# Performance work log

Measured on AMD Instinct MI355X. Metric: run time of the kernel, lower is better.

Reference implementation:

```python
import jax, jax.numpy as jnp
import numpy as np

N_NODES = 8192
N_EDGES = 8192
DEG = 32          # nodes per hyperedge
NNZ = N_EDGES * DEG
D = 32            # embedding_dim / hidden_channels


def setup_inputs() -> dict:
    key = jax.random.key(0)
    ks = jax.random.split(key, 12)
    x_0 = jax.random.normal(ks[0], (N_NODES, D), dtype=jnp.float32)
    # incidence structure: each hyperedge touches DEG random nodes
    node_idx = jax.random.randint(ks[1], (NNZ,), 0, N_NODES)
    edge_idx = jnp.repeat(jnp.arange(N_EDGES), DEG)
    incidence_1 = jnp.zeros((N_NODES, N_EDGES), jnp.float32).at[node_idx, edge_idx].set(1.0)
    s = 1.0 / np.sqrt(D)
    # UniGCN layer weights (level-2 conv linear transform per layer, 2 layers)
    W_l1 = jax.random.uniform(ks[2], (D, D), jnp.float32, -s, s)
    W_l2 = jax.random.uniform(ks[3], (D, D), jnp.float32, -s, s)
    # 3-layer MLP (Linear(64,32), Linear(32,32), Linear(32,1)), no activations
    s2 = 1.0 / np.sqrt(2 * D)
    Wm1 = jax.random.uniform(ks[4], (2 * D, D), jnp.float32, -s2, s2)
    bm1 = jax.random.uniform(ks[5], (D,), jnp.float32, -s2, s2)
    Wm2 = jax.random.uniform(ks[6], (D, D), jnp.float32, -s, s)
    bm2 = jax.random.uniform(ks[7], (D,), jnp.float32, -s, s)
    Wm3 = jax.random.uniform(ks[8], (D, 1), jnp.float32, -s, s)
    bm3 = jax.random.uniform(ks[9], (1,), jnp.float32, -s, s)
    return {"x_0": x_0, "incidence_1": incidence_1,
            "W_l1": W_l1, "W_l2": W_l2,
            "Wm1": Wm1, "bm1": bm1, "Wm2": Wm2, "bm2": bm2,
            "Wm3": Wm3, "bm3": bm3,
            "node_idx": node_idx, "edge_idx": edge_idx}


def _unigcn(x_0, inc, W_l1, W_l2):
    # UniGCN layer: level1 (0->1, no linear transform), level2 (1->0, linear)
    x_1 = inc.T @ x_0                 # [E, D]
    x_0 = inc @ (x_1 @ W_l1)          # [N, D]
    x_1 = inc.T @ x_0                 # [E, D]
    x_0 = inc @ (x_1 @ W_l2)          # [N, D]
    return x_0, x_1


def reference(x_0, incidence_1, W_l1, W_l2, Wm1, bm1, Wm2, bm2, Wm3, bm3,
              node_idx, edge_idx):
    x_0_new, x_1_new = _unigcn(x_0, incidence_1, W_l1, W_l2)
    # gather embeddings at incidence nonzeros
    h = jnp.concatenate([x_0_new[node_idx], x_1_new[edge_idx]], axis=1)  # [NNZ, 2D]
    h = h @ Wm1 + bm1
    h = h @ Wm2 + bm2
    vals = (h @ Wm3 + bm3)[:, 0]                                          # [NNZ]
    # scatter back into dense [N, E] matrix
    output_counts = jnp.zeros_like(incidence_1).at[node_idx, edge_idx].set(vals)
    return output_counts
```

## Files before the change

### kernel.cpp

```cpp
#include <hip/hip_runtime.h>

#define N_NODES 8192
#define N_EDGES 8192
#define DEG 32
#define D 32
#define CAP 128
#define FILL_GRID 2048

typedef float vf4 __attribute__((ext_vector_type(4)));


__global__ void __launch_bounds__(256)
k1_fill(const float* __restrict__ x0, const float* __restrict__ Wl1,
        const float* __restrict__ Wl2, const float* __restrict__ Wm1,
        const float* __restrict__ bm1, const float* __restrict__ Wm2,
        const float* __restrict__ bm2, const float* __restrict__ Wm3,
        const float* __restrict__ bm3, const int* __restrict__ node_idx,
        float* __restrict__ A, unsigned* __restrict__ validmask,
        int* __restrict__ cursor, int* __restrict__ csr_e,
        float* __restrict__ consts, float* __restrict__ out) {
    const int t = threadIdx.x, el = t >> 5, s = t & 31;

    if (blockIdx.x < N_EDGES / 8) {
        __shared__ int sidx[8][32];
        __shared__ unsigned smask[8];
        __shared__ float fsh[128];
        if (blockIdx.x == 0) {
            float* w23 = fsh;
            float* M0  = fsh + 32;
            float* M1  = fsh + 64;
            float* w2u = fsh + 96;
            if (t < 32) {
                float acc = 0.f;
                for (int k = 0; k < 32; ++k) acc += Wm2[t * 32 + k] * Wm3[k];
                w23[t] = acc;
            }
            __syncthreads();
            if (t < 64) {
                float acc = 0.f;
                for (int k = 0; k < 32; ++k) acc += Wm1[t * 32 + k] * w23[k];
                if (t < 32) M0[t] = acc; else M1[t - 32] = acc;
            }
            if (t == 0) {
                float c = bm3[0];
                for (int k = 0; k < 32; ++k) c += bm1[k] * w23[k] + bm2[k] * Wm3[k];
                consts[0] = c;
            }
            __syncthreads();
            if (t < 32) {
                float acc = 0.f;
                for (int d2 = 0; d2 < 32; ++d2) acc += Wl2[t * 32 + d2] * M0[d2];
                w2u[t] = acc;
            }
            __syncthreads();
            if (t < 32) {
                float ay = 0.f, az = 0.f;
                for (int d2 = 0; d2 < 32; ++d2) {
                    float w = Wl1[t * 32 + d2];
                    ay += w * w2u[d2];
                    az += w * M1[d2];
                }
                consts[1 + t]  = ay;
                consts[33 + t] = az;
            }
            __syncthreads();
        }

        int e = blockIdx.x * 8 + el;
        int idx = node_idx[e * DEG + s];
        sidx[el][s] = idx;
        __syncthreads();
        bool valid = true;
        for (int j = 0; j < s; ++j)
            if (sidx[el][j] == idx) { valid = false; break; }
        unsigned long long bl = __ballot(valid);
        if (s == 0) {
            unsigned m = (unsigned)(bl >> (t & 32));
            smask[el] = m;
            validmask[e] = m;
        }
        if (valid) {
            int pos = atomicAdd(&cursor[idx], 1);
            if (pos < CAP) csr_e[idx * CAP + pos] = e;
        }
        __syncthreads();
        unsigned m = smask[el];
        float acc = 0.f;
#pragma unroll
        for (int j = 0; j < 32; ++j)
            if ((m >> j) & 1u) acc += x0[sidx[el][j] * D + s];
        A[e * D + s] = acc;
    }

    vf4* dst = (vf4*)out;
    const long long nvec = (long long)N_NODES * N_EDGES / 4;
    const long long stride = (long long)FILL_GRID * 256;
    vf4 zz = (vf4)(0.f);
    for (long long i = (long long)blockIdx.x * 256 + t; i < nvec; i += stride)
        dst[i] = zz;
}

__global__ void __launch_bounds__(256)
k2_node(const float* __restrict__ A, const int* __restrict__ csr_e,
        const int* __restrict__ cursor, const float* __restrict__ consts,
        float* __restrict__ y, float* __restrict__ z) {
    const int t = threadIdx.x, el = t >> 5, s = t & 31;
    int n = blockIdx.x * 8 + el;
    int cnt = min(cursor[n], CAP);
    const int* lst = csr_e + n * CAP;
    float acc = 0.f;
    int j = 0;
    for (; j + 4 <= cnt; j += 4) {
        int4 e4 = *(const int4*)(lst + j);
        acc += A[e4.x * D + s] + A[e4.y * D + s] +
               A[e4.z * D + s] + A[e4.w * D + s];
    }
    for (; j < cnt; ++j) acc += A[lst[j] * D + s];
    float ay = acc * consts[1 + s];
    float az = acc * consts[33 + s];
#pragma unroll
    for (int off = 16; off; off >>= 1) {
        ay += __shfl_xor(ay, off);
        az += __shfl_xor(az, off);
    }
    if (s == 0) { y[n] = ay; z[n] = az; }
}

__global__ void __launch_bounds__(256)
k2_edge(const int* __restrict__ node_idx, const unsigned* __restrict__ validmask,
        const float* __restrict__ y, const float* __restrict__ z,
        float* __restrict__ qw, float* __restrict__ q) {
    const int t = threadIdx.x, el = t >> 5, s = t & 31;
    int e = blockIdx.x * 8 + el;
    unsigned m = validmask[e];
    int idx = node_idx[e * DEG + s];
    bool valid = (m >> s) & 1u;
    float ay = valid ? y[idx] : 0.f;
    float az = valid ? z[idx] : 0.f;
#pragma unroll
    for (int off = 16; off; off >>= 1) {
        ay += __shfl_xor(ay, off);
        az += __shfl_xor(az, off);
    }
    if (s == 0) { qw[e] = ay; q[e] = az; }
}

__global__ void __launch_bounds__(256)
k_patch(const int* __restrict__ csr_e, const int* __restrict__ cursor,
        const float* __restrict__ qw, const float* __restrict__ q,
        const float* __restrict__ consts, float* __restrict__ out) {
    const int t = threadIdx.x, el = t >> 5, s = t & 31;
    int n = blockIdx.x * 8 + el;
    int cnt = min(cursor[n], CAP);
    const int* lst = csr_e + n * CAP;
    float acc = 0.f;
    for (int j = s; j < cnt; j += 32) acc += qw[lst[j]];
#pragma unroll
    for (int off = 16; off; off >>= 1) acc += __shfl_xor(acc, off);
    float pn = acc + consts[0];
    float* rowp = out + (size_t)n * N_EDGES;
    for (int j = s; j < cnt; j += 32) {
        int e = lst[j];
        rowp[e] = pn + q[e];
    }
}

extern "C" void kernel_launch(void* const* d_in, const int* in_sizes, int n_in,
                              void* d_out, int out_size, void* d_ws, size_t ws_size,
                              hipStream_t stream) {
    const float* x0  = (const float*)d_in[0];
    const float* Wl1 = (const float*)d_in[2];
    const float* Wl2 = (const float*)d_in[3];
    const float* Wm1 = (const float*)d_in[4];
    const float* bm1 = (const float*)d_in[5];
    const float* Wm2 = (const float*)d_in[6];
    const float* bm2 = (const float*)d_in[7];
    const float* Wm3 = (const float*)d_in[8];
    const float* bm3 = (const float*)d_in[9];
    const int* node_idx = (const int*)d_in[10];
    float* out = (float*)d_out;

    char* ws = (char*)d_ws;
    int*      cursor    = (int*)(ws);
    float*    y         = (float*)(ws + ( 32u << 10));
    float*    z         = (float*)(ws + ( 64u << 10));
    unsigned* validmask = (unsigned*)(ws + ( 96u << 10));
    float*    qw        = (float*)(ws + (128u << 10));
    float*    q         = (float*)(ws + (160u << 10));
    float*    consts    = (float*)(ws + (192u << 10));
    float*    A         = (float*)(ws + (1u << 20));
    int*      csr_e     = (int*)(ws + (2u << 20));

    hipMemsetAsync(cursor, 0, N_NODES * sizeof(int), stream);
    k1_fill<<<FILL_GRID, 256, 0, stream>>>(x0, Wl1, Wl2, Wm1, bm1, Wm2, bm2,
                                           Wm3, bm3, node_idx, A, validmask,
                                           cursor, csr_e, consts, out);
    k2_node<<<N_NODES / 8, 256, 0, stream>>>(A, csr_e, cursor, consts, y, z);
    k2_edge<<<N_EDGES / 8, 256, 0, stream>>>(node_idx, validmask, y, z, qw, q);
    k_patch<<<N_NODES / 8, 256, 0, stream>>>(csr_e, cursor, qw, q, consts, out);
}
```

Before: 82.40 us.

## Move output zero-fill from first kernel into per-row patch kernel

The dense 256MB output zero-fill is moved out of the first kernel, where it ran grid-strided alongside the edge/CSR work. It now lives in the final patch kernel, where each block zeroes 4 full rows and then scatters the nonzero values into those same rows. Rows are written while still hot in cache, and the first kernel becomes a small edge-only launch. The cost is that the fill no longer overlaps the edge, node and edge-reduce stages, and only 4 of 8 warps do the patch work.

```diff
diff --git a/kernel.cpp b/kernel.cpp
--- a/kernel.cpp
+++ b/kernel.cpp
@@ -5,99 +5,90 @@
 #define DEG 32
 #define D 32
 #define CAP 128
-#define FILL_GRID 2048
+#define ROWS_PER_BLK 4
 
 typedef float vf4 __attribute__((ext_vector_type(4)));
 
 
 __global__ void __launch_bounds__(256)
-k1_fill(const float* __restrict__ x0, const float* __restrict__ Wl1,
+k1_edge(const float* __restrict__ x0, const float* __restrict__ Wl1,
         const float* __restrict__ Wl2, const float* __restrict__ Wm1,
         const float* __restrict__ bm1, const float* __restrict__ Wm2,
         const float* __restrict__ bm2, const float* __restrict__ Wm3,
         const float* __restrict__ bm3, const int* __restrict__ node_idx,
         float* __restrict__ A, unsigned* __restrict__ validmask,
         int* __restrict__ cursor, int* __restrict__ csr_e,
-        float* __restrict__ consts, float* __restrict__ out) {
+        float* __restrict__ consts) {
+    __shared__ int sidx[8][32];
+    __shared__ unsigned smask[8];
+    __shared__ float fsh[128];
     const int t = threadIdx.x, el = t >> 5, s = t & 31;
 
-    if (blockIdx.x < N_EDGES / 8) {
-        __shared__ int sidx[8][32];
-        __shared__ unsigned smask[8];
-        __shared__ float fsh[128];
-        if (blockIdx.x == 0) {
-            float* w23 = fsh;
-            float* M0  = fsh + 32;
-            float* M1  = fsh + 64;
-            float* w2u = fsh + 96;
-            if (t < 32) {
-                float acc = 0.f;
-                for (int k = 0; k < 32; ++k) acc += Wm2[t * 32 + k] * Wm3[k];
-                w23[t] = acc;
+    if (blockIdx.x == 0) {
+        float* w23 = fsh;
+        float* M0  = fsh + 32;
+        float* M1  = fsh + 64;
+        float* w2u = fsh + 96;
+        if (t < 32) {
+            float acc = 0.f;
+            for (int k = 0; k < 32; ++k) acc += Wm2[t * 32 + k] * Wm3[k];
+            w23[t] = acc;
+        }
+        __syncthreads();
+        if (t < 64) {
+            float acc = 0.f;
+            for (int k = 0; k < 32; ++k) acc += Wm1[t * 32 + k] * w23[k];
+            if (t < 32) M0[t] = acc; else M1[t - 32] = acc;
+        }
+        if (t == 0) {
+            float c = bm3[0];
+            for (int k = 0; k < 32; ++k) c += bm1[k] * w23[k] + bm2[k] * Wm3[k];
+            consts[0] = c;
+        }
+        __syncthreads();
+        if (t < 32) {
+            float acc = 0.f;
+            for (int d2 = 0; d2 < 32; ++d2) acc += Wl2[t * 32 + d2] * M0[d2];
+            w2u[t] = acc;
+        }
+        __syncthreads();
+        if (t < 32) {
+            float ay = 0.f, az = 0.f;
+            for (int d2 = 0; d2 < 32; ++d2) {
+                float w = Wl1[t * 32 + d2];
+                ay += w * w2u[d2];
+                az += w * M1[d2];
             }
-            __syncthreads();
-            if (t < 64) {
-                float acc = 0.f;
-                for (int k = 0; k < 32; ++k) acc += Wm1[t * 32 + k] * w23[k];
-                if (t < 32) M0[t] = acc; else M1[t - 32] = acc;
-            }
-            if (t == 0) {
-                float c = bm3[0];
-                for (int k = 0; k < 32; ++k) c += bm1[k] * w23[k] + bm2[k] * Wm3[k];
-                consts[0] = c;
-            }
-            __syncthreads();
-            if (t < 32) {
-                float acc = 0.f;
-                for (int d2 = 0; d2 < 32; ++d2) acc += Wl2[t * 32 + d2] * M0[d2];
-                w2u[t] = acc;
-            }
-            __syncthreads();
-            if (t < 32) {
-                float ay = 0.f, az = 0.f;
-                for (int d2 = 0; d2 < 32; ++d2) {
-                    float w = Wl1[t * 32 + d2];
-                    ay += w * w2u[d2];
-                    az += w * M1[d2];
-                }
-                consts[1 + t]  = ay;
-                consts[33 + t] = az;
-            }
-            __syncthreads();
-        }
-
-        int e = blockIdx.x * 8 + el;
-        int idx = node_idx[e * DEG + s];
-        sidx[el][s] = idx;
-        __syncthreads();
-        bool valid = true;
-        for (int j = 0; j < s; ++j)
-            if (sidx[el][j] == idx) { valid = false; break; }
-        unsigned long long bl = __ballot(valid);
-        if (s == 0) {
-            unsigned m = (unsigned)(bl >> (t & 32));
-            smask[el] = m;
-            validmask[e] = m;
-        }
-        if (valid) {
-            int pos = atomicAdd(&cursor[idx], 1);
-            if (pos < CAP) csr_e[idx * CAP + pos] = e;
-        }
-        __syncthreads();
-        unsigned m = smask[el];
-        float acc = 0.f;
-#pragma unroll
-        for (int j = 0; j < 32; ++j)
-            if ((m >> j) & 1u) acc += x0[sidx[el][j] * D + s];
-        A[e * D + s] = acc;
-    }
-
-    vf4* dst = (vf4*)out;
-    const long long nvec = (long long)N_NODES * N_EDGES / 4;
-    const long long stride = (long long)FILL_GRID * 256;
-    vf4 zz = (vf4)(0.f);
-    for (long long i = (long long)blockIdx.x * 256 + t; i < nvec; i += stride)
-        dst[i] = zz;
+            consts[1 + t]  = ay;
+            consts[33 + t] = az;
+        }
+        __syncthreads();
+    }
+
+    int e = blockIdx.x * 8 + el;
+    int idx = node_idx[e * DEG + s];
+    sidx[el][s] = idx;
+    __syncthreads();
+    bool valid = true;
+    for (int j = 0; j < s; ++j)
+        if (sidx[el][j] == idx) { valid = false; break; }
+    unsigned long long bl = __ballot(valid);
+    if (s == 0) {
+        unsigned m = (unsigned)(bl >> (t & 32));
+        smask[el] = m;
+        validmask[e] = m;
+    }
+    if (valid) {
+        int pos = atomicAdd(&cursor[idx], 1);
+        if (pos < CAP) csr_e[idx * CAP + pos] = e;
+    }
+    __syncthreads();
+    unsigned m = smask[el];
+    float acc = 0.f;
+#pragma unroll
+    for (int j = 0; j < 32; ++j)
+        if ((m >> j) & 1u) acc += x0[sidx[el][j] * D + s];
+    A[e * D + s] = acc;
 }
 
 __global__ void __launch_bounds__(256)
@@ -146,22 +137,33 @@
 }
 
 __global__ void __launch_bounds__(256)
-k_patch(const int* __restrict__ csr_e, const int* __restrict__ cursor,
-        const float* __restrict__ qw, const float* __restrict__ q,
-        const float* __restrict__ consts, float* __restrict__ out) {
-    const int t = threadIdx.x, el = t >> 5, s = t & 31;
-    int n = blockIdx.x * 8 + el;
-    int cnt = min(cursor[n], CAP);
-    const int* lst = csr_e + n * CAP;
-    float acc = 0.f;
-    for (int j = s; j < cnt; j += 32) acc += qw[lst[j]];
-#pragma unroll
-    for (int off = 16; off; off >>= 1) acc += __shfl_xor(acc, off);
-    float pn = acc + consts[0];
-    float* rowp = out + (size_t)n * N_EDGES;
-    for (int j = s; j < cnt; j += 32) {
-        int e = lst[j];
-        rowp[e] = pn + q[e];
+k_fillpatch(const int* __restrict__ csr_e, const int* __restrict__ cursor,
+            const float* __restrict__ qw, const float* __restrict__ q,
+            const float* __restrict__ consts, float* __restrict__ out) {
+    const int t = threadIdx.x, w = t >> 5, s = t & 31;
+    const int n0 = blockIdx.x * ROWS_PER_BLK;
+
+    vf4* dst = (vf4*)(out + (size_t)n0 * N_EDGES);
+    vf4 zz = (vf4)(0.f);
+#pragma unroll
+    for (int k = 0; k < 32; ++k)
+        dst[t + 256 * k] = zz;
+    __syncthreads();
+
+    if (w < ROWS_PER_BLK) {
+        int n = n0 + w;
+        int cnt = min(cursor[n], CAP);
+        const int* lst = csr_e + n * CAP;
+        float acc = 0.f;
+        for (int j = s; j < cnt; j += 32) acc += qw[lst[j]];
+#pragma unroll
+        for (int off = 16; off; off >>= 1) acc += __shfl_xor(acc, off);
+        float pn = acc + consts[0];
+        float* rowp = out + (size_t)n * N_EDGES;
+        for (int j = s; j < cnt; j += 32) {
+            int e = lst[j];
+            rowp[e] = pn + q[e];
+        }
     }
 }
 
@@ -192,10 +194,11 @@
     int*      csr_e     = (int*)(ws + (2u << 20));
 
     hipMemsetAsync(cursor, 0, N_NODES * sizeof(int), stream);
-    k1_fill<<<FILL_GRID, 256, 0, stream>>>(x0, Wl1, Wl2, Wm1, bm1, Wm2, bm2,
-                                           Wm3, bm3, node_idx, A, validmask,
-                                           cursor, csr_e, consts, out);
+    k1_edge<<<N_EDGES / 8, 256, 0, stream>>>(x0, Wl1, Wl2, Wm1, bm1, Wm2, bm2,
+                                             Wm3, bm3, node_idx, A, validmask,
+                                             cursor, csr_e, consts);
     k2_node<<<N_NODES / 8, 256, 0, stream>>>(A, csr_e, cursor, consts, y, z);
     k2_edge<<<N_EDGES / 8, 256, 0, stream>>>(node_idx, validmask, y, z, qw, q);
-    k_patch<<<N_NODES / 8, 256, 0, stream>>>(csr_e, cursor, qw, q, consts, out);
-}
+    k_fillpatch<<<N_NODES / ROWS_PER_BLK, 256, 0, stream>>>(csr_e, cursor, qw, q,
+                                                            consts, out);
+}
```

Measured after the change: 86.46 us. +4.9%, slower.
